# Optimization experiments

Hardware: AMD Instinct MI355X
Metric: run time of the kernel (lower is better)

The kernel has to match this reference:

```python
import jax, jax.numpy as jnp
import numpy as np

B, H, N = 256, 128, 2048

def setup_inputs() -> dict:
    key = jax.random.key(0)
    k1, k2, k3, k4, k5 = jax.random.split(key, 5)
    return {
        "static_hidden": jax.random.normal(k1, (B, H, N), dtype=jnp.float32),
        "dynamic_hidden": jax.random.normal(k2, (B, H, N), dtype=jnp.float32),
        "decoder_hidden": jax.random.normal(k3, (B, H), dtype=jnp.float32),
        "v": jax.random.normal(k4, (1, 1, H), dtype=jnp.float32) * 0.05,
        "W": jax.random.normal(k5, (1, H, 3 * H), dtype=jnp.float32) * 0.05,
    }

def reference(static_hidden, dynamic_hidden, decoder_hidden, v, W):
    # hidden: [B, 3H, N] = concat(static, dynamic, broadcast(decoder))
    dec = jnp.broadcast_to(decoder_hidden[:, :, None], static_hidden.shape)
    hidden = jnp.concatenate((static_hidden, dynamic_hidden, dec), axis=1)
    # W @ hidden: [B, H, N]; tanh; v @ .: [B, 1, N]
    Wh = jnp.tanh(jnp.einsum('hk,bkn->bhn', W[0], hidden))
    scores = jnp.einsum('h,bhn->bn', v[0, 0], Wh)[:, None, :]  # [B,1,N]
    return jax.nn.softmax(scores, axis=2)
```

## Files before the change

kernel.cpp:

```cpp
#include <hip/hip_runtime.h>
#include <cstddef>

#define Bn 256
#define Hd 128
#define Nd 2048
#define K3 384
#define K2 256

typedef _Float16 half8 __attribute__((ext_vector_type(8)));
typedef float    float4v __attribute__((ext_vector_type(4)));

__device__ __forceinline__ float fast_tanh(float x) {
    return 1.0f - __fdividef(2.0f, __expf(2.0f * x) + 1.0f);
}

__global__ void prep_w16(const float* __restrict__ W, _Float16* __restrict__ Wf) {
    int idx = blockIdx.x * 256 + threadIdx.x;
    int h = idx >> 8, k = idx & 255;
    Wf[idx] = (_Float16)W[h * K3 + k];
}

__global__ void prep_c(const float* __restrict__ W, const float* __restrict__ dec,
                       float* __restrict__ cb) {
    __shared__ float dl[Hd];
    int b = blockIdx.x;
    int h = threadIdx.x;
    dl[h] = dec[b * Hd + h];
    __syncthreads();
    float acc = 0.f;
    #pragma unroll 8
    for (int k = 0; k < Hd; ++k)
        acc = fmaf(W[h * K3 + 256 + k], dl[k], acc);
    cb[b * Hd + h] = acc;
}

__global__ __launch_bounds__(512, 4)
void score_kernel(const float* __restrict__ shp, const float* __restrict__ dhp,
                  const _Float16* __restrict__ Wf, const float* __restrict__ cbp,
                  const float* __restrict__ v, float* __restrict__ out) {
    __shared__ __align__(16) _Float16 xl[128 * 256];
    __shared__ float red[4 * 128];

    const int tid  = threadIdx.x;
    const int w    = __builtin_amdgcn_readfirstlane(tid >> 6);
    const int lane = tid & 63;
    const int qd   = lane >> 4;
    const int ln   = lane & 15;
    const int b    = blockIdx.y;
    const int n0   = blockIdx.x * 128;

    {
        const int hf = lane >> 5;
        const int L  = lane & 31;
        const int n  = 4 * L;
        const float* base = (w < 4)
            ? shp + (size_t)b * (Hd * (size_t)Nd) + (size_t)(32 * w) * Nd + n0 + n
            : dhp + (size_t)b * (Hd * (size_t)Nd) + (size_t)(32 * w - 128) * Nd + n0 + n;

        float4v xv[2][8];
        #pragma unroll
        for (int t = 0; t < 2; ++t)
            #pragma unroll
            for (int j = 0; j < 8; ++j)
                xv[t][j] = *reinterpret_cast<const float4v*>(
                    base + (size_t)(16 * t + 8 * hf + j) * Nd);

        #pragma unroll
        for (int t = 0; t < 2; ++t) {
            const int ck = 4 * w + 2 * t + hf;
            #pragma unroll
            for (int r = 0; r < 4; ++r) {
                half8 e;
                #pragma unroll
                for (int j = 0; j < 8; ++j) e[j] = (_Float16)xv[t][j][r];
                const int row = n + r;
                const int p = ck ^ ((row >> 1) & 7);
                *reinterpret_cast<half8*>(&xl[row * 256 + p * 8]) = e;
            }
        }
    }
    __syncthreads();

    const int mh = w & 3;
    const int nh = w >> 2;
    const int h0 = mh * 32;
    const int swr = (ln >> 1) & 7;

    float4v acc[2][4];
    #pragma unroll
    for (int Mt = 0; Mt < 2; ++Mt) {
        float4v c4 = *reinterpret_cast<const float4v*>(cbp + b * Hd + h0 + Mt * 16 + qd * 4);
        #pragma unroll
        for (int Nt = 0; Nt < 4; ++Nt) acc[Mt][Nt] = c4;
    }

    const _Float16* wp0 = Wf + ((h0 + ln) << 8) + qd * 8;
    const _Float16* wp1 = Wf + ((h0 + 16 + ln) << 8) + qd * 8;
    half8 a0 = *reinterpret_cast<const half8*>(wp0);
    half8 a1 = *reinterpret_cast<const half8*>(wp1);
    #pragma unroll
    for (int kt = 0; kt < 8; ++kt) {
        half8 a0n, a1n;
        if (kt < 7) {
            a0n = *reinterpret_cast<const half8*>(wp0 + (kt + 1) * 32);
            a1n = *reinterpret_cast<const half8*>(wp1 + (kt + 1) * 32);
        }
        half8 Bf[4];
        const int ckb = kt * 4 + qd;
        #pragma unroll
        for (int Nt = 0; Nt < 4; ++Nt) {
            const int row = nh * 64 + Nt * 16 + ln;
            Bf[Nt] = *reinterpret_cast<const half8*>(&xl[row * 256 + ((ckb ^ swr) << 3)]);
        }
        #pragma unroll
        for (int Nt = 0; Nt < 4; ++Nt) {
            acc[0][Nt] = __builtin_amdgcn_mfma_f32_16x16x32_f16(a0, Bf[Nt], acc[0][Nt], 0, 0, 0);
            acc[1][Nt] = __builtin_amdgcn_mfma_f32_16x16x32_f16(a1, Bf[Nt], acc[1][Nt], 0, 0, 0);
        }
        if (kt < 7) { a0 = a0n; a1 = a1n; }
    }

    float4v v0 = *reinterpret_cast<const float4v*>(v + h0 + qd * 4);
    float4v v1 = *reinterpret_cast<const float4v*>(v + h0 + 16 + qd * 4);
    #pragma unroll
    for (int Nt = 0; Nt < 4; ++Nt) {
        float part = 0.f;
        #pragma unroll
        for (int r = 0; r < 4; ++r) {
            part = fmaf(v0[r], fast_tanh(acc[0][Nt][r]), part);
            part = fmaf(v1[r], fast_tanh(acc[1][Nt][r]), part);
        }
        part += __shfl_xor(part, 16);
        part += __shfl_xor(part, 32);
        if (qd == 0) red[mh * 128 + nh * 64 + Nt * 16 + ln] = part;
    }
    __syncthreads();
    if (tid < 128) {
        float s = red[tid] + red[128 + tid] + red[256 + tid] + red[384 + tid];
        out[(size_t)b * Nd + n0 + tid] = s;
    }
}

__global__ void softmax_k(float* __restrict__ out) {
    int b = blockIdx.x;
    float* row = out + (size_t)b * Nd;
    int tid = threadIdx.x;

    float loc[8];
    float mx = -3.4e38f;
    #pragma unroll
    for (int i = 0; i < 8; ++i) {
        loc[i] = row[tid + (i << 8)];
        mx = fmaxf(mx, loc[i]);
    }
    #pragma unroll
    for (int off = 32; off > 0; off >>= 1) mx = fmaxf(mx, __shfl_xor(mx, off));
    __shared__ float s4[4];
    if ((tid & 63) == 0) s4[tid >> 6] = mx;
    __syncthreads();
    mx = fmaxf(fmaxf(s4[0], s4[1]), fmaxf(s4[2], s4[3]));

    float sum = 0.f;
    #pragma unroll
    for (int i = 0; i < 8; ++i) {
        loc[i] = __expf(loc[i] - mx);
        sum += loc[i];
    }
    #pragma unroll
    for (int off = 32; off > 0; off >>= 1) sum += __shfl_xor(sum, off);
    __shared__ float s4b[4];
    if ((tid & 63) == 0) s4b[tid >> 6] = sum;
    __syncthreads();
    sum = s4b[0] + s4b[1] + s4b[2] + s4b[3];

    float inv = 1.0f / sum;
    #pragma unroll
    for (int i = 0; i < 8; ++i) row[tid + (i << 8)] = loc[i] * inv;
}

extern "C" void kernel_launch(void* const* d_in, const int* in_sizes, int n_in,
                              void* d_out, int out_size, void* d_ws, size_t ws_size,
                              hipStream_t stream) {
    const float* shp = (const float*)d_in[0];
    const float* dhp = (const float*)d_in[1];
    const float* dec = (const float*)d_in[2];
    const float* v   = (const float*)d_in[3];
    const float* W   = (const float*)d_in[4];
    float* out = (float*)d_out;

    _Float16* Wf = (_Float16*)d_ws;
    float* cbp = (float*)((char*)d_ws + 65536);

    hipLaunchKernelGGL(prep_w16, dim3(128), dim3(256), 0, stream, W, Wf);
    hipLaunchKernelGGL(prep_c,   dim3(Bn),  dim3(Hd),  0, stream, W, dec, cbp);
    hipLaunchKernelGGL(score_kernel, dim3(Nd / 128, Bn), dim3(512), 0, stream,
                       shp, dhp, Wf, cbp, v, out);
    hipLaunchKernelGGL(softmax_k, dim3(Bn), dim3(256), 0, stream, out);
}
```

Measured before the change: 556.3 us.

## Overlap dynamic-hidden loads with static-half MFMAs using 4-wave blocks

```diff
diff --git a/kernel.cpp b/kernel.cpp
--- a/kernel.cpp
+++ b/kernel.cpp
@@ -5,10 +5,11 @@
 #define Hd 128
 #define Nd 2048
 #define K3 384
-#define K2 256
 
 typedef _Float16 half8 __attribute__((ext_vector_type(8)));
 typedef float    float4v __attribute__((ext_vector_type(4)));
+
+#define SFENCE() __builtin_amdgcn_sched_barrier(0)
 
 __device__ __forceinline__ float fast_tanh(float x) {
     return 1.0f - __fdividef(2.0f, __expf(2.0f * x) + 1.0f);
@@ -34,7 +35,7 @@
     cb[b * Hd + h] = acc;
 }
 
-__global__ __launch_bounds__(512, 4)
+__global__ __launch_bounds__(256, 2)
 void score_kernel(const float* __restrict__ shp, const float* __restrict__ dhp,
                   const _Float16* __restrict__ Wf, const float* __restrict__ cbp,
                   const float* __restrict__ v, float* __restrict__ out) {
@@ -48,82 +49,119 @@
     const int ln   = lane & 15;
     const int b    = blockIdx.y;
     const int n0   = blockIdx.x * 128;
-
-    {
-        const int hf = lane >> 5;
-        const int L  = lane & 31;
-        const int n  = 4 * L;
-        const float* base = (w < 4)
-            ? shp + (size_t)b * (Hd * (size_t)Nd) + (size_t)(32 * w) * Nd + n0 + n
-            : dhp + (size_t)b * (Hd * (size_t)Nd) + (size_t)(32 * w - 128) * Nd + n0 + n;
-
-        float4v xv[2][8];
-        #pragma unroll
-        for (int t = 0; t < 2; ++t)
-            #pragma unroll
-            for (int j = 0; j < 8; ++j)
-                xv[t][j] = *reinterpret_cast<const float4v*>(
-                    base + (size_t)(16 * t + 8 * hf + j) * Nd);
-
-        #pragma unroll
-        for (int t = 0; t < 2; ++t) {
-            const int ck = 4 * w + 2 * t + hf;
-            #pragma unroll
-            for (int r = 0; r < 4; ++r) {
-                half8 e;
-                #pragma unroll
-                for (int j = 0; j < 8; ++j) e[j] = (_Float16)xv[t][j][r];
-                const int row = n + r;
-                const int p = ck ^ ((row >> 1) & 7);
-                *reinterpret_cast<half8*>(&xl[row * 256 + p * 8]) = e;
-            }
-        }
-    }
-    __syncthreads();
-
-    const int mh = w & 3;
-    const int nh = w >> 2;
-    const int h0 = mh * 32;
-    const int swr = (ln >> 1) & 7;
-
-    float4v acc[2][4];
+    const int h0   = w * 32;
+
+    half8 Af[2][8];
+    #pragma unroll
+    for (int Mt = 0; Mt < 2; ++Mt) {
+        const _Float16* wp = Wf + ((h0 + Mt * 16 + ln) << 8) + qd * 8;
+        #pragma unroll
+        for (int kt = 0; kt < 8; ++kt)
+            Af[Mt][kt] = *reinterpret_cast<const half8*>(wp + kt * 32);
+    }
+
+    float4v acc[2][8];
     #pragma unroll
     for (int Mt = 0; Mt < 2; ++Mt) {
         float4v c4 = *reinterpret_cast<const float4v*>(cbp + b * Hd + h0 + Mt * 16 + qd * 4);
         #pragma unroll
-        for (int Nt = 0; Nt < 4; ++Nt) acc[Mt][Nt] = c4;
-    }
-
-    const _Float16* wp0 = Wf + ((h0 + ln) << 8) + qd * 8;
-    const _Float16* wp1 = Wf + ((h0 + 16 + ln) << 8) + qd * 8;
-    half8 a0 = *reinterpret_cast<const half8*>(wp0);
-    half8 a1 = *reinterpret_cast<const half8*>(wp1);
-    #pragma unroll
-    for (int kt = 0; kt < 8; ++kt) {
-        half8 a0n, a1n;
-        if (kt < 7) {
-            a0n = *reinterpret_cast<const half8*>(wp0 + (kt + 1) * 32);
-            a1n = *reinterpret_cast<const half8*>(wp1 + (kt + 1) * 32);
-        }
-        half8 Bf[4];
+        for (int Nt = 0; Nt < 8; ++Nt) acc[Mt][Nt] = c4;
+    }
+
+    const int n1  = 2 * lane;
+    const int swz = lane & 7;
+    const size_t bofs = (size_t)b * (Hd * (size_t)Nd) + n0 + n1;
+
+    {
+        const float* src = shp + bofs;
+        #pragma unroll
+        for (int i = 0; i < 4; ++i) {
+            const int kl = i * 32 + w * 8;
+            float2 xv[8];
+            #pragma unroll
+            for (int j = 0; j < 8; ++j)
+                xv[j] = *reinterpret_cast<const float2*>(src + (size_t)(kl + j) * Nd);
+            half8 e0, e1;
+            #pragma unroll
+            for (int j = 0; j < 8; ++j) {
+                e0[j] = (_Float16)xv[j].x;
+                e1[j] = (_Float16)xv[j].y;
+            }
+            const int p = (kl >> 3) ^ swz;
+            *reinterpret_cast<half8*>(&xl[n1 * 256 + p * 8])       = e0;
+            *reinterpret_cast<half8*>(&xl[(n1 + 1) * 256 + p * 8]) = e1;
+        }
+    }
+    __syncthreads();
+
+    const int swr = (ln >> 1) & 7;
+    const float* dsrc = dhp + bofs;
+
+    #pragma unroll
+    for (int hp = 0; hp < 2; ++hp) {
+        float2 yv[2][8];
+        #pragma unroll
+        for (int i2 = 0; i2 < 2; ++i2) {
+            const int kl = (2 * hp + i2) * 32 + w * 8;
+            #pragma unroll
+            for (int j = 0; j < 8; ++j)
+                yv[i2][j] = *reinterpret_cast<const float2*>(dsrc + (size_t)(kl + j) * Nd);
+        }
+        SFENCE();
+
+        #pragma unroll
+        for (int kt = 2 * hp; kt < 2 * hp + 2; ++kt) {
+            half8 Bf[8];
+            const int ckb = kt * 4 + qd;
+            #pragma unroll
+            for (int Nt = 0; Nt < 8; ++Nt) {
+                const int row = Nt * 16 + ln;
+                Bf[Nt] = *reinterpret_cast<const half8*>(&xl[row * 256 + ((ckb ^ swr) << 3)]);
+            }
+            #pragma unroll
+            for (int Nt = 0; Nt < 8; ++Nt) {
+                acc[0][Nt] = __builtin_amdgcn_mfma_f32_16x16x32_f16(Af[0][kt], Bf[Nt], acc[0][Nt], 0, 0, 0);
+                acc[1][Nt] = __builtin_amdgcn_mfma_f32_16x16x32_f16(Af[1][kt], Bf[Nt], acc[1][Nt], 0, 0, 0);
+            }
+        }
+        SFENCE();
+
+        #pragma unroll
+        for (int i2 = 0; i2 < 2; ++i2) {
+            const int kl = (2 * hp + i2) * 32 + w * 8;
+            half8 e0, e1;
+            #pragma unroll
+            for (int j = 0; j < 8; ++j) {
+                e0[j] = (_Float16)yv[i2][j].x;
+                e1[j] = (_Float16)yv[i2][j].y;
+            }
+            const int p = ((128 + kl) >> 3) ^ swz;
+            *reinterpret_cast<half8*>(&xl[n1 * 256 + p * 8])       = e0;
+            *reinterpret_cast<half8*>(&xl[(n1 + 1) * 256 + p * 8]) = e1;
+        }
+    }
+    __syncthreads();
+
+    #pragma unroll
+    for (int kt = 4; kt < 8; ++kt) {
+        half8 Bf[8];
         const int ckb = kt * 4 + qd;
         #pragma unroll
-        for (int Nt = 0; Nt < 4; ++Nt) {
-            const int row = nh * 64 + Nt * 16 + ln;
+        for (int Nt = 0; Nt < 8; ++Nt) {
+            const int row = Nt * 16 + ln;
             Bf[Nt] = *reinterpret_cast<const half8*>(&xl[row * 256 + ((ckb ^ swr) << 3)]);
         }
         #pragma unroll
-        for (int Nt = 0; Nt < 4; ++Nt) {
-            acc[0][Nt] = __builtin_amdgcn_mfma_f32_16x16x32_f16(a0, Bf[Nt], acc[0][Nt], 0, 0, 0);
-            acc[1][Nt] = __builtin_amdgcn_mfma_f32_16x16x32_f16(a1, Bf[Nt], acc[1][Nt], 0, 0, 0);
-        }
-        if (kt < 7) { a0 = a0n; a1 = a1n; }
+        for (int Nt = 0; Nt < 8; ++Nt) {
+            acc[0][Nt] = __builtin_amdgcn_mfma_f32_16x16x32_f16(Af[0][kt], Bf[Nt], acc[0][Nt], 0, 0, 0);
+            acc[1][Nt] = __builtin_amdgcn_mfma_f32_16x16x32_f16(Af[1][kt], Bf[Nt], acc[1][Nt], 0, 0, 0);
+        }
     }
 
     float4v v0 = *reinterpret_cast<const float4v*>(v + h0 + qd * 4);
     float4v v1 = *reinterpret_cast<const float4v*>(v + h0 + 16 + qd * 4);
     #pragma unroll
-    for (int Nt = 0; Nt < 4; ++Nt) {
+    for (int Nt = 0; Nt < 8; ++Nt) {
         float part = 0.f;
         #pragma unroll
         for (int r = 0; r < 4; ++r) {
@@ -132,7 +170,7 @@
         }
         part += __shfl_xor(part, 16);
         part += __shfl_xor(part, 32);
-        if (qd == 0) red[mh * 128 + nh * 64 + Nt * 16 + ln] = part;
+        if (qd == 0) red[w * 128 + Nt * 16 + ln] = part;
     }
     __syncthreads();
     if (tid < 128) {
@@ -193,7 +231,7 @@
 
     hipLaunchKernelGGL(prep_w16, dim3(128), dim3(256), 0, stream, W, Wf);
     hipLaunchKernelGGL(prep_c,   dim3(Bn),  dim3(Hd),  0, stream, W, dec, cbp);
-    hipLaunchKernelGGL(score_kernel, dim3(Nd / 128, Bn), dim3(512), 0, stream,
+    hipLaunchKernelGGL(score_kernel, dim3(Nd / 128, Bn), dim3(256), 0, stream,
                        shp, dhp, Wf, cbp, v, out);
     hipLaunchKernelGGL(softmax_k, dim3(Bn), dim3(256), 0, stream, out);
 }
```

New measurement: 515.1 us, median of 2. -7.4%, faster.

## Shrink score tile to 64 columns and overlap dynamic loads with static MFMA

Applied to the files above, without the earlier changes.

```diff
diff --git a/kernel.cpp b/kernel.cpp
--- a/kernel.cpp
+++ b/kernel.cpp
@@ -5,10 +5,12 @@
 #define Hd 128
 #define Nd 2048
 #define K3 384
-#define K2 256
+#define NT 64
 
 typedef _Float16 half8 __attribute__((ext_vector_type(8)));
 typedef float    float4v __attribute__((ext_vector_type(4)));
+
+#define SFENCE() __builtin_amdgcn_sched_barrier(0)
 
 __device__ __forceinline__ float fast_tanh(float x) {
     return 1.0f - __fdividef(2.0f, __expf(2.0f * x) + 1.0f);
@@ -34,12 +36,12 @@
     cb[b * Hd + h] = acc;
 }
 
-__global__ __launch_bounds__(512, 4)
+__global__ __launch_bounds__(256, 4)
 void score_kernel(const float* __restrict__ shp, const float* __restrict__ dhp,
                   const _Float16* __restrict__ Wf, const float* __restrict__ cbp,
                   const float* __restrict__ v, float* __restrict__ out) {
-    __shared__ __align__(16) _Float16 xl[128 * 256];
-    __shared__ float red[4 * 128];
+    __shared__ __align__(16) _Float16 xl[NT * 256];
+    __shared__ float red[4 * NT];
 
     const int tid  = threadIdx.x;
     const int w    = __builtin_amdgcn_readfirstlane(tid >> 6);
@@ -47,81 +49,99 @@
     const int qd   = lane >> 4;
     const int ln   = lane & 15;
     const int b    = blockIdx.y;
-    const int n0   = blockIdx.x * 128;
-
+    const int n0   = blockIdx.x * NT;
+    const int h0   = w * 32;
+    const size_t bstr = (size_t)Hd * Nd;
+
+    float4v acc[2][4];
     {
-        const int hf = lane >> 5;
-        const int L  = lane & 31;
-        const int n  = 4 * L;
-        const float* base = (w < 4)
-            ? shp + (size_t)b * (Hd * (size_t)Nd) + (size_t)(32 * w) * Nd + n0 + n
-            : dhp + (size_t)b * (Hd * (size_t)Nd) + (size_t)(32 * w - 128) * Nd + n0 + n;
-
-        float4v xv[2][8];
-        #pragma unroll
-        for (int t = 0; t < 2; ++t)
+        float4v c0 = *reinterpret_cast<const float4v*>(cbp + (size_t)b * Hd + h0 + qd * 4);
+        float4v c1 = *reinterpret_cast<const float4v*>(cbp + (size_t)b * Hd + h0 + 16 + qd * 4);
+        #pragma unroll
+        for (int Nt = 0; Nt < 4; ++Nt) { acc[0][Nt] = c0; acc[1][Nt] = c1; }
+    }
+
+    half8 A[4][2];
+    #pragma unroll
+    for (int kt = 0; kt < 4; ++kt) {
+        A[kt][0] = *reinterpret_cast<const half8*>(Wf + ((h0 + ln) << 8) + kt * 32 + qd * 8);
+        A[kt][1] = *reinterpret_cast<const half8*>(Wf + ((h0 + 16 + ln) << 8) + kt * 32 + qd * 8);
+    }
+
+    const float* sb = shp + (size_t)b * bstr + n0 + 4 * ln;
+    const float* db = dhp + (size_t)b * bstr + n0 + 4 * ln;
+    float4v t[8];
+    {
+        #pragma unroll
+        for (int j = 0; j < 8; ++j)
+            t[j] = *reinterpret_cast<const float4v*>(sb + (size_t)(32 * w + 8 * qd + j) * Nd);
+        const int ck = 4 * w + qd;
+        #pragma unroll
+        for (int r = 0; r < 4; ++r) {
+            const int n  = 4 * ln + r;
+            const int sw = (n >> 1) & 7;
+            half8 e;
             #pragma unroll
-            for (int j = 0; j < 8; ++j)
-                xv[t][j] = *reinterpret_cast<const float4v*>(
-                    base + (size_t)(16 * t + 8 * hf + j) * Nd);
-
-        #pragma unroll
-        for (int t = 0; t < 2; ++t) {
-            const int ck = 4 * w + 2 * t + hf;
+            for (int j = 0; j < 8; ++j) e[j] = (_Float16)t[j][r];
+            *reinterpret_cast<half8*>(&xl[n * 256 + ((ck ^ sw) << 3)]) = e;
+        }
+    }
+    __syncthreads();
+
+    const int swr = (ln >> 1) & 7;
+
+    SFENCE();
+    #pragma unroll
+    for (int j = 0; j < 8; ++j)
+        t[j] = *reinterpret_cast<const float4v*>(db + (size_t)(32 * w + 8 * qd + j) * Nd);
+    SFENCE();
+
+    #pragma unroll
+    for (int kt = 0; kt < 4; ++kt) {
+        const int ckb = kt * 4 + qd;
+        #pragma unroll
+        for (int Nt = 0; Nt < 4; ++Nt) {
+            const int row = Nt * 16 + ln;
+            half8 Bf = *reinterpret_cast<const half8*>(&xl[row * 256 + ((ckb ^ swr) << 3)]);
+            acc[0][Nt] = __builtin_amdgcn_mfma_f32_16x16x32_f16(A[kt][0], Bf, acc[0][Nt], 0, 0, 0);
+            acc[1][Nt] = __builtin_amdgcn_mfma_f32_16x16x32_f16(A[kt][1], Bf, acc[1][Nt], 0, 0, 0);
+        }
+    }
+    SFENCE();
+
+    {
+        const int ck = 16 + 4 * w + qd;
+        #pragma unroll
+        for (int r = 0; r < 4; ++r) {
+            const int n  = 4 * ln + r;
+            const int sw = (n >> 1) & 7;
+            half8 e;
             #pragma unroll
-            for (int r = 0; r < 4; ++r) {
-                half8 e;
-                #pragma unroll
-                for (int j = 0; j < 8; ++j) e[j] = (_Float16)xv[t][j][r];
-                const int row = n + r;
-                const int p = ck ^ ((row >> 1) & 7);
-                *reinterpret_cast<half8*>(&xl[row * 256 + p * 8]) = e;
-            }
-        }
-    }
-    __syncthreads();
-
-    const int mh = w & 3;
-    const int nh = w >> 2;
-    const int h0 = mh * 32;
-    const int swr = (ln >> 1) & 7;
-
-    float4v acc[2][4];
-    #pragma unroll
-    for (int Mt = 0; Mt < 2; ++Mt) {
-        float4v c4 = *reinterpret_cast<const float4v*>(cbp + b * Hd + h0 + Mt * 16 + qd * 4);
-        #pragma unroll
-        for (int Nt = 0; Nt < 4; ++Nt) acc[Mt][Nt] = c4;
-    }
-
-    const _Float16* wp0 = Wf + ((h0 + ln) << 8) + qd * 8;
-    const _Float16* wp1 = Wf + ((h0 + 16 + ln) << 8) + qd * 8;
-    half8 a0 = *reinterpret_cast<const half8*>(wp0);
-    half8 a1 = *reinterpret_cast<const half8*>(wp1);
-    #pragma unroll
-    for (int kt = 0; kt < 8; ++kt) {
-        half8 a0n, a1n;
-        if (kt < 7) {
-            a0n = *reinterpret_cast<const half8*>(wp0 + (kt + 1) * 32);
-            a1n = *reinterpret_cast<const half8*>(wp1 + (kt + 1) * 32);
-        }
-        half8 Bf[4];
-        const int ckb = kt * 4 + qd;
+            for (int j = 0; j < 8; ++j) e[j] = (_Float16)t[j][r];
+            *reinterpret_cast<half8*>(&xl[n * 256 + ((ck ^ sw) << 3)]) = e;
+        }
+    }
+    __syncthreads();
+
+    #pragma unroll
+    for (int kt = 0; kt < 4; ++kt) {
+        A[kt][0] = *reinterpret_cast<const half8*>(Wf + ((h0 + ln) << 8) + (kt + 4) * 32 + qd * 8);
+        A[kt][1] = *reinterpret_cast<const half8*>(Wf + ((h0 + 16 + ln) << 8) + (kt + 4) * 32 + qd * 8);
+    }
+    #pragma unroll
+    for (int kt = 0; kt < 4; ++kt) {
+        const int ckb = (kt + 4) * 4 + qd;
         #pragma unroll
         for (int Nt = 0; Nt < 4; ++Nt) {
-            const int row = nh * 64 + Nt * 16 + ln;
-            Bf[Nt] = *reinterpret_cast<const half8*>(&xl[row * 256 + ((ckb ^ swr) << 3)]);
-        }
-        #pragma unroll
-        for (int Nt = 0; Nt < 4; ++Nt) {
-            acc[0][Nt] = __builtin_amdgcn_mfma_f32_16x16x32_f16(a0, Bf[Nt], acc[0][Nt], 0, 0, 0);
-            acc[1][Nt] = __builtin_amdgcn_mfma_f32_16x16x32_f16(a1, Bf[Nt], acc[1][Nt], 0, 0, 0);
-        }
-        if (kt < 7) { a0 = a0n; a1 = a1n; }
-    }
-
-    float4v v0 = *reinterpret_cast<const float4v*>(v + h0 + qd * 4);
-    float4v v1 = *reinterpret_cast<const float4v*>(v + h0 + 16 + qd * 4);
+            const int row = Nt * 16 + ln;
+            half8 Bf = *reinterpret_cast<const half8*>(&xl[row * 256 + ((ckb ^ swr) << 3)]);
+            acc[0][Nt] = __builtin_amdgcn_mfma_f32_16x16x32_f16(A[kt][0], Bf, acc[0][Nt], 0, 0, 0);
+            acc[1][Nt] = __builtin_amdgcn_mfma_f32_16x16x32_f16(A[kt][1], Bf, acc[1][Nt], 0, 0, 0);
+        }
+    }
+
+    const float4v v0 = *reinterpret_cast<const float4v*>(v + h0 + qd * 4);
+    const float4v v1 = *reinterpret_cast<const float4v*>(v + h0 + 16 + qd * 4);
     #pragma unroll
     for (int Nt = 0; Nt < 4; ++Nt) {
         float part = 0.f;
@@ -132,11 +152,11 @@
         }
         part += __shfl_xor(part, 16);
         part += __shfl_xor(part, 32);
-        if (qd == 0) red[mh * 128 + nh * 64 + Nt * 16 + ln] = part;
-    }
-    __syncthreads();
-    if (tid < 128) {
-        float s = red[tid] + red[128 + tid] + red[256 + tid] + red[384 + tid];
+        if (qd == 0) red[w * NT + Nt * 16 + ln] = part;
+    }
+    __syncthreads();
+    if (tid < NT) {
+        float s = red[tid] + red[NT + tid] + red[2 * NT + tid] + red[3 * NT + tid];
         out[(size_t)b * Nd + n0 + tid] = s;
     }
 }
@@ -193,7 +213,7 @@
 
     hipLaunchKernelGGL(prep_w16, dim3(128), dim3(256), 0, stream, W, Wf);
     hipLaunchKernelGGL(prep_c,   dim3(Bn),  dim3(Hd),  0, stream, W, dec, cbp);
-    hipLaunchKernelGGL(score_kernel, dim3(Nd / 128, Bn), dim3(512), 0, stream,
+    hipLaunchKernelGGL(score_kernel, dim3(Nd / NT, Bn), dim3(256), 0, stream,
                        shp, dhp, Wf, cbp, v, out);
     hipLaunchKernelGGL(softmax_k, dim3(Bn), dim3(256), 0, stream, out);
 }
```

Measured after the change: 534.5 us. -3.9%, faster.
